# Kernel tuning notes

Hardware: AMD Instinct MI355X
Metric: run time of the kernel (lower is better)

## Reference

```python
import jax, jax.numpy as jnp
import numpy as np

N_WAY = 100
K_SHOT = 10
N_SUPPORT = N_WAY * K_SHOT
N_QUERY = 8192
F_IN = 4096
D_EMB = 1024
EPS = 1e-6  # torch nn.PairwiseDistance default eps added to the difference


def setup_inputs() -> dict:
    key = jax.random.key(0)
    k1, k2, k3, k4 = jax.random.split(key, 4)
    support_images = jax.random.normal(k1, (N_SUPPORT, F_IN), dtype=jnp.float32)
    # dense labels 0..N_WAY-1, K_SHOT examples each (episodic sampling)
    support_labels = (jnp.arange(N_SUPPORT, dtype=jnp.int32) // K_SHOT)
    query_images = jax.random.normal(k2, (N_QUERY, F_IN), dtype=jnp.float32)
    W = jax.random.normal(k3, (F_IN, D_EMB), dtype=jnp.float32) * (1.0 / np.sqrt(F_IN))
    b = jax.random.normal(k4, (D_EMB,), dtype=jnp.float32) * 0.01
    return {"support_images": support_images, "support_labels": support_labels,
            "query_images": query_images, "W": W, "b": b}


def reference(support_images, support_labels, query_images, W, b):
    # backbone: linear feature extractor
    z_support = support_images @ W + b          # [N_SUPPORT, D]
    z_query = query_images @ W + b              # [N_QUERY, D]

    # group support embeddings by class (each class has exactly K_SHOT members)
    order = jnp.argsort(support_labels, stable=True)
    grouped = z_support[order].reshape(N_WAY, K_SHOT, D_EMB)  # [W, K, D]

    # torch .median(dim=0): lower median for even counts -> sorted[(K-1)//2]
    z_proto_med = jnp.sort(grouped, axis=1)[:, (K_SHOT - 1) // 2]  # [W, D]
    z_proto_mean = grouped.mean(axis=1)                            # [W, D]
    z_total = 0.5 * (z_proto_med + z_proto_mean)                   # [W, D]

    # pairwise L2 with torch PairwiseDistance eps: sqrt(sum((q - p + eps)^2))
    # expanded: ||q||^2 + ||p||^2 + D*eps^2 - 2 q.p + 2*eps*(sum q - sum p)
    q2 = jnp.sum(z_query * z_query, axis=-1, keepdims=True)       # [Q, 1]
    p2 = jnp.sum(z_total * z_total, axis=-1)[None, :]             # [1, W]
    qs = jnp.sum(z_query, axis=-1, keepdims=True)                 # [Q, 1]
    ps = jnp.sum(z_total, axis=-1)[None, :]                       # [1, W]
    cross = z_query @ z_total.T                                   # [Q, W]
    sq = q2 + p2 - 2.0 * cross + 2.0 * EPS * (qs - ps) + D_EMB * EPS * EPS
    dists = jnp.sqrt(jnp.maximum(sq, 0.0))                        # [Q, W]
    return -dists
```

## Files before the change

### kernel.cpp

```cpp
#include <hip/hip_runtime.h>


typedef unsigned short u16;
typedef __attribute__((ext_vector_type(4))) unsigned short u16x4;
typedef __attribute__((ext_vector_type(8))) unsigned short u16x8;
typedef __attribute__((ext_vector_type(8))) short bf16x8;
typedef __attribute__((ext_vector_type(4))) float f32x4;

#define N_QUERY 8192
#define F_IN    4096
#define D_EMB   1024
#define N_SUP   1000
#define N_WAY   100
#define BK      64
#define BM      96

__device__ __forceinline__ u16 f2b(float f) {
  unsigned int u = __builtin_bit_cast(unsigned int, f);
  u += 0x7FFFu + ((u >> 16) & 1u);
  return (u16)(u >> 16);
}
__device__ __forceinline__ float b2f(u16 u) {
  unsigned int x = ((unsigned int)u) << 16;
  return __builtin_bit_cast(float, x);
}

#define GLB_PTR(p) ((const __attribute__((address_space(1))) unsigned int*)(p))
#define LDS_PTR(p) ((__attribute__((address_space(3))) unsigned int*)(p))

__global__ __launch_bounds__(256) void wt_k(const float* __restrict__ W,
                                            u16* __restrict__ Wt) {
  __shared__ float tile[32][33];
  int kb = blockIdx.x * 32, nb = blockIdx.y * 32;
  int tx = threadIdx.x & 31, ty = threadIdx.x >> 5;
#pragma unroll
  for (int i = 0; i < 4; ++i) {
    int k = ty + i * 8;
    tile[k][tx] = W[(size_t)(kb + k) * D_EMB + nb + tx];
  }
  __syncthreads();
#pragma unroll
  for (int i = 0; i < 4; ++i) {
    int n = ty + i * 8;
    Wt[(size_t)(nb + n) * F_IN + kb + tx] = f2b(tile[tx][n]);
  }
}

__global__ __launch_bounds__(512) void gemm1_k(
    const float* __restrict__ qimg, const float* __restrict__ simg,
    const u16* __restrict__ Wt, const float* __restrict__ bias,
    u16* __restrict__ Zq) {
  __shared__ __align__(16) u16 As[BM * BK];
  __shared__ __align__(16) u16 Bs[128 * BK];
  const int tid  = threadIdx.x;
  const int lane = tid & 63, wid = tid >> 6;
  const int wr = wid >> 2, wc = wid & 3;
  int lin = blockIdx.x + (blockIdx.y << 3);
  int swz = (lin & 7) * 96 + (lin >> 3);
  const int rowBase = (swz >> 3) * BM;
  const int colBase = (swz & 7) * 128;
  const bool a2 = (tid < 256);

  const float* asrc[2];
  int aw[2];
#pragma unroll
  for (int i = 0; i < 2; ++i) {
    int g = i * 512 + tid;
    if (g > 767) g = 767;
    int row = g >> 3;
    int colb = ((g & 7) << 4) ^ ((row & 7) << 4);
    int grow = rowBase + row;
    int sr = grow - N_QUERY; if (sr < 0) sr = 0; if (sr > N_SUP - 1) sr = N_SUP - 1;
    const float* base = (grow < N_QUERY) ? qimg + (size_t)grow * F_IN
                                         : simg + (size_t)sr * F_IN;
    asrc[i] = base + (colb >> 1);
    aw[i] = g * 8;
  }
  const u16* bsrc[2];
  unsigned bldsoff[2];
#pragma unroll
  for (int i = 0; i < 2; ++i) {
    int g = i * 512 + tid;
    int n = g >> 3;
    int kb = ((g & 7) << 4) ^ ((n & 7) << 4);
    bsrc[i] = Wt + (size_t)(colBase + n) * F_IN + (kb >> 1);
    bldsoff[i] = i * 8192 + wid * 1024;
  }
  int aoff[3], boff[2];
#pragma unroll
  for (int m = 0; m < 3; ++m) {
    int row = wr * 48 + m * 16 + (lane & 15);
    aoff[m] = (row * 128 + (((lane >> 4) << 4) ^ ((row & 7) << 4))) >> 1;
  }
#pragma unroll
  for (int n = 0; n < 2; ++n) {
    int row = wc * 32 + n * 16 + (lane & 15);
    boff[n] = (row * 128 + (((lane >> 4) << 4) ^ ((row & 7) << 4))) >> 1;
  }

  f32x4 acc[3][2] = {};

#pragma unroll 1
  for (int kt = 0; kt < F_IN / BK; ++kt) {
    float4 v0a = *(const float4*)(asrc[0] + kt * BK);
    float4 v0b = *(const float4*)(asrc[0] + kt * BK + 4);
    float4 v1a = {}, v1b = {};
    if (a2) {
      v1a = *(const float4*)(asrc[1] + kt * BK);
      v1b = *(const float4*)(asrc[1] + kt * BK + 4);
    }
#pragma unroll
    for (int i = 0; i < 2; ++i)
      __builtin_amdgcn_global_load_lds(GLB_PTR(bsrc[i] + kt * BK),
                                       LDS_PTR((char*)Bs + bldsoff[i]), 16, 0, 0);
    u16x8 pk0 = { f2b(v0a.x), f2b(v0a.y), f2b(v0a.z), f2b(v0a.w),
                  f2b(v0b.x), f2b(v0b.y), f2b(v0b.z), f2b(v0b.w) };
    *(u16x8*)&As[aw[0]] = pk0;
    if (a2) {
      u16x8 pk1 = { f2b(v1a.x), f2b(v1a.y), f2b(v1a.z), f2b(v1a.w),
                    f2b(v1b.x), f2b(v1b.y), f2b(v1b.z), f2b(v1b.w) };
      *(u16x8*)&As[aw[1]] = pk1;
    }
    __syncthreads();

#pragma unroll
    for (int ks = 0; ks < 2; ++ks) {
      bf16x8 a[3], b[2];
#pragma unroll
      for (int m = 0; m < 3; ++m) a[m] = *(const bf16x8*)&As[aoff[m] ^ (ks << 5)];
#pragma unroll
      for (int n = 0; n < 2; ++n) b[n] = *(const bf16x8*)&Bs[boff[n] ^ (ks << 5)];
#pragma unroll
      for (int m = 0; m < 3; ++m)
#pragma unroll
        for (int n = 0; n < 2; ++n)
          acc[m][n] = __builtin_amdgcn_mfma_f32_16x16x32_bf16(a[m], b[n], acc[m][n], 0, 0, 0);
    }
    __syncthreads();
  }

#pragma unroll
  for (int n = 0; n < 2; ++n) {
    int c = colBase + wc * 32 + n * 16 + (lane & 15);
    float bvv = bias[c];
#pragma unroll
    for (int m = 0; m < 3; ++m) {
      int r0 = rowBase + wr * 48 + m * 16 + ((lane >> 4) * 4);
#pragma unroll
      for (int r = 0; r < 4; ++r)
        Zq[(size_t)(r0 + r) * D_EMB + c] = f2b(acc[m][n][r] + bvv);
    }
  }
}

__global__ __launch_bounds__(256) void proto_k(const u16* __restrict__ Zq,
                                               float* __restrict__ Ztf) {
  int gid = blockIdx.x * 256 + threadIdx.x;
  int w = gid >> 10, d = gid & 1023;
  float outv = 0.f;
  if (w < N_WAY) {
    float v[10]; float s = 0.f;
#pragma unroll
    for (int k = 0; k < 10; ++k) {
      v[k] = b2f(Zq[(size_t)(N_QUERY + w * 10 + k) * D_EMB + d]);
      s += v[k];
    }
#pragma unroll
    for (int a = 0; a < 9; ++a)
#pragma unroll
      for (int b2 = 0; b2 < 9; ++b2)
        if (b2 < 9 - a) {
          float lo = fminf(v[b2], v[b2 + 1]);
          float hi = fmaxf(v[b2], v[b2 + 1]);
          v[b2] = lo; v[b2 + 1] = hi;
        }
    outv = 0.5f * (v[4] + s * 0.1f);
  }
  Ztf[gid] = outv;
}

__global__ __launch_bounds__(256) void stats_k(const float* __restrict__ in,
                                               u16* __restrict__ outb,
                                               float* __restrict__ sum2,
                                               float* __restrict__ sum1) {
  int row = blockIdx.x;
  const float* r = in + (size_t)row * D_EMB;
  int t = threadIdx.x;
  float4 v = *(const float4*)(r + t * 4);
  u16x4 u4 = { f2b(v.x), f2b(v.y), f2b(v.z), f2b(v.w) };
  *(u16x4*)(outb + (size_t)row * D_EMB + t * 4) = u4;
  float s  = v.x + v.y + v.z + v.w;
  float s2 = v.x * v.x + v.y * v.y + v.z * v.z + v.w * v.w;
#pragma unroll
  for (int off = 32; off > 0; off >>= 1) {
    s  += __shfl_down(s, off);
    s2 += __shfl_down(s2, off);
  }
  __shared__ float as1[4], as2[4];
  if ((t & 63) == 0) { as1[t >> 6] = s; as2[t >> 6] = s2; }
  __syncthreads();
  if (t == 0) {
    sum1[row] = as1[0] + as1[1] + as1[2] + as1[3];
    sum2[row] = as2[0] + as2[1] + as2[2] + as2[3];
  }
}

#define LDA2 40
__global__ __launch_bounds__(256) void gemm2_k(
    const u16* __restrict__ Zq, const u16* __restrict__ Ztb,
    const float* __restrict__ p2, const float* __restrict__ ps,
    float* __restrict__ out) {
  __shared__ u16 As[16][LDA2];
  __shared__ u16 Bs[128][LDA2];
  __shared__ float q2_l[16], qs_l[16];
  const int tid = threadIdx.x;
  const int lane = tid & 63, wid = tid >> 6;
  const int wc = wid;
  const int rowBase = blockIdx.x * 16;
  const bool stA = (tid < 64);

  f32x4 acc[2] = {};
  float rs = 0.f, rs2 = 0.f;

  for (int kt = 0; kt < D_EMB / 32; ++kt) {
    u16x8 avv = {};
    if (stA) {
      int row = tid >> 2, kh = tid & 3;
      avv = *(const u16x8*)(Zq + (size_t)(rowBase + row) * D_EMB + kt * 32 + kh * 8);
    }
    u16x8 bvv[2];
#pragma unroll
    for (int i = 0; i < 2; ++i) {
      int u = i * 256 + tid;
      int n = u >> 2, kh = u & 3;
      bvv[i] = *(const u16x8*)(Ztb + (size_t)n * D_EMB + kt * 32 + kh * 8);
    }
    __syncthreads();
    if (stA) {
      int row = tid >> 2, kh = tid & 3;
      *(u16x8*)&As[row][kh * 8] = avv;
#pragma unroll
      for (int j = 0; j < 8; ++j) {
        float x = b2f(avv[j]);
        rs += x; rs2 += x * x;
      }
    }
#pragma unroll
    for (int i = 0; i < 2; ++i) {
      int u = i * 256 + tid;
      int n = u >> 2, kh = u & 3;
      *(u16x8*)&Bs[n][kh * 8] = bvv[i];
    }
    __syncthreads();

    bf16x8 a, b[2];
    a = *(const bf16x8*)&As[lane & 15][(lane >> 4) * 8];
#pragma unroll
    for (int n = 0; n < 2; ++n)
      b[n] = *(const bf16x8*)&Bs[wc * 32 + n * 16 + (lane & 15)][(lane >> 4) * 8];
#pragma unroll
    for (int n = 0; n < 2; ++n)
      acc[n] = __builtin_amdgcn_mfma_f32_16x16x32_bf16(a, b[n], acc[n], 0, 0, 0);
    __syncthreads();
  }

  rs  += __shfl_down(rs, 1);  rs  += __shfl_down(rs, 2);
  rs2 += __shfl_down(rs2, 1); rs2 += __shfl_down(rs2, 2);
  if (stA && (tid & 3) == 0) {
    qs_l[tid >> 2] = rs;
    q2_l[tid >> 2] = rs2;
  }
  __syncthreads();

  {
    int r0 = (lane >> 4) * 4;
    float q2v[4], qsv[4];
#pragma unroll
    for (int r = 0; r < 4; ++r) { q2v[r] = q2_l[r0 + r]; qsv[r] = qs_l[r0 + r]; }
#pragma unroll
    for (int n = 0; n < 2; ++n) {
      int c = wc * 32 + n * 16 + (lane & 15);
      if (c < N_WAY) {
        float pp = p2[c], pss = ps[c];
#pragma unroll
        for (int r = 0; r < 4; ++r) {
          float sq = q2v[r] + pp - 2.f * acc[n][r]
                   + 2e-6f * (qsv[r] - pss) + (float)D_EMB * 1e-12f;
          out[(size_t)(rowBase + r0 + r) * N_WAY + c] = -sqrtf(fmaxf(sq, 0.f));
        }
      }
    }
  }
}

extern "C" void kernel_launch(void* const* d_in, const int* in_sizes, int n_in,
                              void* d_out, int out_size, void* d_ws, size_t ws_size,
                              hipStream_t stream) {
  const float* simg = (const float*)d_in[0];
  const float* qimg = (const float*)d_in[2];
  const float* W    = (const float*)d_in[3];
  const float* bias = (const float*)d_in[4];
  float* out = (float*)d_out;

  char* ws = (char*)d_ws;
  u16*   Wt  = (u16*)(ws);
  u16*   Zq  = (u16*)(ws + 8388608);
  float* Ztf = (float*)(ws + 27262976);
  u16*   Ztb = (u16*)(ws + 27787264);
  float* p2  = (float*)(ws + 28114944);
  float* ps  = (float*)(ws + 28115456);

  hipLaunchKernelGGL(wt_k,    dim3(128, 32), dim3(256), 0, stream, W, Wt);
  hipLaunchKernelGGL(gemm1_k, dim3(8, 96),   dim3(512), 0, stream, qimg, simg, Wt, bias, Zq);
  hipLaunchKernelGGL(proto_k, dim3(512),     dim3(256), 0, stream, Zq, Ztf);
  hipLaunchKernelGGL(stats_k, dim3(128),     dim3(256), 0, stream, Ztf, Ztb, p2, ps);
  hipLaunchKernelGGL(gemm2_k, dim3(512),     dim3(256), 0, stream, Zq, Ztb, p2, ps, out);
}
```

Baseline: 138.9 us.

## Switch projection GEMM to 32x32x16 MFMA with 64x128 tiles and 256 threads

Rewrites the first GEMM to use 32x32x16 bf16 MFMA instructions, with each of four waves computing a 32x64 output tile. The block tile shrinks from 96x128 to 64x128, and the grid grows from 768 to 1152 blocks of 256 threads. Larger MFMA shapes cut the number of LDS fragment reads per FLOP and remove the idle-thread branch in the A load. The cost is less B reuse per block, more blocks re-reading W, and a different LDS access pattern.

```diff
diff --git a/kernel.cpp b/kernel.cpp
--- a/kernel.cpp
+++ b/kernel.cpp
@@ -6,6 +6,7 @@
 typedef __attribute__((ext_vector_type(8))) unsigned short u16x8;
 typedef __attribute__((ext_vector_type(8))) short bf16x8;
 typedef __attribute__((ext_vector_type(4))) float f32x4;
+typedef __attribute__((ext_vector_type(16))) float f32x16;
 
 #define N_QUERY 8192
 #define F_IN    4096
@@ -13,7 +14,6 @@
 #define N_SUP   1000
 #define N_WAY   100
 #define BK      64
-#define BM      96
 
 __device__ __forceinline__ u16 f2b(float f) {
   unsigned int u = __builtin_bit_cast(unsigned int, f);
@@ -46,27 +46,25 @@
   }
 }
 
-__global__ __launch_bounds__(512) void gemm1_k(
+__global__ __launch_bounds__(256) void gemm1_k(
     const float* __restrict__ qimg, const float* __restrict__ simg,
     const u16* __restrict__ Wt, const float* __restrict__ bias,
     u16* __restrict__ Zq) {
-  __shared__ __align__(16) u16 As[BM * BK];
+  __shared__ __align__(16) u16 As[64 * BK];
   __shared__ __align__(16) u16 Bs[128 * BK];
   const int tid  = threadIdx.x;
   const int lane = tid & 63, wid = tid >> 6;
-  const int wr = wid >> 2, wc = wid & 3;
+  const int wr = wid >> 1, wc = wid & 1;
   int lin = blockIdx.x + (blockIdx.y << 3);
-  int swz = (lin & 7) * 96 + (lin >> 3);
-  const int rowBase = (swz >> 3) * BM;
+  int swz = (lin & 7) * 144 + (lin >> 3);
+  const int rowBase = (swz >> 3) * 64;
   const int colBase = (swz & 7) * 128;
-  const bool a2 = (tid < 256);
 
   const float* asrc[2];
   int aw[2];
 #pragma unroll
   for (int i = 0; i < 2; ++i) {
-    int g = i * 512 + tid;
-    if (g > 767) g = 767;
+    int g = i * 256 + tid;
     int row = g >> 3;
     int colb = ((g & 7) << 4) ^ ((row & 7) << 4);
     int grow = rowBase + row;
@@ -76,79 +74,75 @@
     asrc[i] = base + (colb >> 1);
     aw[i] = g * 8;
   }
-  const u16* bsrc[2];
-  unsigned bldsoff[2];
-#pragma unroll
-  for (int i = 0; i < 2; ++i) {
-    int g = i * 512 + tid;
+  const u16* bsrc[4];
+  unsigned bldsoff[4];
+#pragma unroll
+  for (int i = 0; i < 4; ++i) {
+    int g = i * 256 + tid;
     int n = g >> 3;
     int kb = ((g & 7) << 4) ^ ((n & 7) << 4);
     bsrc[i] = Wt + (size_t)(colBase + n) * F_IN + (kb >> 1);
-    bldsoff[i] = i * 8192 + wid * 1024;
-  }
-  int aoff[3], boff[2];
-#pragma unroll
-  for (int m = 0; m < 3; ++m) {
-    int row = wr * 48 + m * 16 + (lane & 15);
-    aoff[m] = (row * 128 + (((lane >> 4) << 4) ^ ((row & 7) << 4))) >> 1;
-  }
-#pragma unroll
-  for (int n = 0; n < 2; ++n) {
-    int row = wc * 32 + n * 16 + (lane & 15);
-    boff[n] = (row * 128 + (((lane >> 4) << 4) ^ ((row & 7) << 4))) >> 1;
-  }
-
-  f32x4 acc[3][2] = {};
+    bldsoff[i] = i * 4096 + wid * 1024;
+  }
+  int aoff[4], boff[2][4];
+  {
+    int arow = wr * 32 + (lane & 31);
+#pragma unroll
+    for (int ks = 0; ks < 4; ++ks) {
+      int koff = ks * 32 + ((lane >> 5) << 4);
+      aoff[ks] = (arow * 128 + (koff ^ ((arow & 7) << 4))) >> 1;
+    }
+#pragma unroll
+    for (int nb = 0; nb < 2; ++nb) {
+      int brow = wc * 64 + nb * 32 + (lane & 31);
+#pragma unroll
+      for (int ks = 0; ks < 4; ++ks) {
+        int koff = ks * 32 + ((lane >> 5) << 4);
+        boff[nb][ks] = (brow * 128 + (koff ^ ((brow & 7) << 4))) >> 1;
+      }
+    }
+  }
+
+  f32x16 acc0 = {}, acc1 = {};
 
 #pragma unroll 1
   for (int kt = 0; kt < F_IN / BK; ++kt) {
-    float4 v0a = *(const float4*)(asrc[0] + kt * BK);
-    float4 v0b = *(const float4*)(asrc[0] + kt * BK + 4);
-    float4 v1a = {}, v1b = {};
-    if (a2) {
-      v1a = *(const float4*)(asrc[1] + kt * BK);
-      v1b = *(const float4*)(asrc[1] + kt * BK + 4);
-    }
-#pragma unroll
-    for (int i = 0; i < 2; ++i)
+    float4 v00 = *(const float4*)(asrc[0] + kt * BK);
+    float4 v01 = *(const float4*)(asrc[0] + kt * BK + 4);
+    float4 v10 = *(const float4*)(asrc[1] + kt * BK);
+    float4 v11 = *(const float4*)(asrc[1] + kt * BK + 4);
+#pragma unroll
+    for (int i = 0; i < 4; ++i)
       __builtin_amdgcn_global_load_lds(GLB_PTR(bsrc[i] + kt * BK),
                                        LDS_PTR((char*)Bs + bldsoff[i]), 16, 0, 0);
-    u16x8 pk0 = { f2b(v0a.x), f2b(v0a.y), f2b(v0a.z), f2b(v0a.w),
-                  f2b(v0b.x), f2b(v0b.y), f2b(v0b.z), f2b(v0b.w) };
+    u16x8 pk0 = { f2b(v00.x), f2b(v00.y), f2b(v00.z), f2b(v00.w),
+                  f2b(v01.x), f2b(v01.y), f2b(v01.z), f2b(v01.w) };
+    u16x8 pk1 = { f2b(v10.x), f2b(v10.y), f2b(v10.z), f2b(v10.w),
+                  f2b(v11.x), f2b(v11.y), f2b(v11.z), f2b(v11.w) };
     *(u16x8*)&As[aw[0]] = pk0;
-    if (a2) {
-      u16x8 pk1 = { f2b(v1a.x), f2b(v1a.y), f2b(v1a.z), f2b(v1a.w),
-                    f2b(v1b.x), f2b(v1b.y), f2b(v1b.z), f2b(v1b.w) };
-      *(u16x8*)&As[aw[1]] = pk1;
-    }
-    __syncthreads();
-
-#pragma unroll
-    for (int ks = 0; ks < 2; ++ks) {
-      bf16x8 a[3], b[2];
-#pragma unroll
-      for (int m = 0; m < 3; ++m) a[m] = *(const bf16x8*)&As[aoff[m] ^ (ks << 5)];
-#pragma unroll
-      for (int n = 0; n < 2; ++n) b[n] = *(const bf16x8*)&Bs[boff[n] ^ (ks << 5)];
-#pragma unroll
-      for (int m = 0; m < 3; ++m)
-#pragma unroll
-        for (int n = 0; n < 2; ++n)
-          acc[m][n] = __builtin_amdgcn_mfma_f32_16x16x32_bf16(a[m], b[n], acc[m][n], 0, 0, 0);
-    }
-    __syncthreads();
-  }
-
-#pragma unroll
-  for (int n = 0; n < 2; ++n) {
-    int c = colBase + wc * 32 + n * 16 + (lane & 15);
+    *(u16x8*)&As[aw[1]] = pk1;
+    __syncthreads();
+
+#pragma unroll
+    for (int ks = 0; ks < 4; ++ks) {
+      bf16x8 a = *(const bf16x8*)&As[aoff[ks]];
+      bf16x8 b0 = *(const bf16x8*)&Bs[boff[0][ks]];
+      bf16x8 b1 = *(const bf16x8*)&Bs[boff[1][ks]];
+      acc0 = __builtin_amdgcn_mfma_f32_32x32x16_bf16(a, b0, acc0, 0, 0, 0);
+      acc1 = __builtin_amdgcn_mfma_f32_32x32x16_bf16(a, b1, acc1, 0, 0, 0);
+    }
+    __syncthreads();
+  }
+
+#pragma unroll
+  for (int nb = 0; nb < 2; ++nb) {
+    int c = colBase + wc * 64 + nb * 32 + (lane & 31);
     float bvv = bias[c];
-#pragma unroll
-    for (int m = 0; m < 3; ++m) {
-      int r0 = rowBase + wr * 48 + m * 16 + ((lane >> 4) * 4);
-#pragma unroll
-      for (int r = 0; r < 4; ++r)
-        Zq[(size_t)(r0 + r) * D_EMB + c] = f2b(acc[m][n][r] + bvv);
+    const f32x16* ac = nb ? &acc1 : &acc0;
+#pragma unroll
+    for (int j = 0; j < 16; ++j) {
+      int rl = (j & 3) + 8 * (j >> 2) + 4 * (lane >> 5);
+      Zq[(size_t)(rowBase + wr * 32 + rl) * D_EMB + c] = f2b((*ac)[j] + bvv);
     }
   }
 }
@@ -311,7 +305,7 @@
   float* ps  = (float*)(ws + 28115456);
 
   hipLaunchKernelGGL(wt_k,    dim3(128, 32), dim3(256), 0, stream, W, Wt);
-  hipLaunchKernelGGL(gemm1_k, dim3(8, 96),   dim3(512), 0, stream, qimg, simg, Wt, bias, Zq);
+  hipLaunchKernelGGL(gemm1_k, dim3(8, 144),  dim3(256), 0, stream, qimg, simg, Wt, bias, Zq);
   hipLaunchKernelGGL(proto_k, dim3(512),     dim3(256), 0, stream, Zq, Ztf);
   hipLaunchKernelGGL(stats_k, dim3(128),     dim3(256), 0, stream, Ztf, Ztb, p2, ps);
   hipLaunchKernelGGL(gemm2_k, dim3(512),     dim3(256), 0, stream, Zq, Ztb, p2, ps, out);
```

Result: slower. 195.6 us (+40.8%).
